# Kernel optimization log

Hardware: AMD Instinct MI355X
Metric: run time of the kernel (lower is better)

## Reference

```python
import jax, jax.numpy as jnp
import numpy as np

N_GROUP = 4
TOPK_GROUP = 2
TOP_K = 6
ROUTED_SCALE = 2.0

T, H, E, I = 1024, 1024, 16, 704
SHARED_I = 2 * H  # n_shared_experts * hidden_size


def setup_inputs() -> dict:
    key = jax.random.key(0)
    ks = jax.random.split(key, 10)
    s = 0.02
    return {
        "h": jax.random.normal(ks[0], (T, H), jnp.float32),
        "gate_w": jax.random.normal(ks[1], (E, H), jnp.float32) * s,
        "bias": jax.random.normal(ks[2], (E,), jnp.float32) * 0.1,
        "wg": jax.random.normal(ks[3], (E, H, I), jnp.float32) * s,
        "wu": jax.random.normal(ks[4], (E, H, I), jnp.float32) * s,
        "wd": jax.random.normal(ks[5], (E, I, H), jnp.float32) * s,
        "swg": jax.random.normal(ks[6], (H, SHARED_I), jnp.float32) * s,
        "swu": jax.random.normal(ks[7], (H, SHARED_I), jnp.float32) * s,
        "swd": jax.random.normal(ks[8], (SHARED_I, H), jnp.float32) * s,
    }


def _moe_forward(h, gate_w, bias, wg, wu, wd, swg, swu, swd):
    Tn, Hd = h.shape
    En = gate_w.shape[0]
    per_group = En // N_GROUP

    # shared expert (SwiGLU MLP)
    shared = (jax.nn.silu(h @ swg) * (h @ swu)) @ swd  # [T, H]

    # gate: noaux_tc biased grouped top-k routing (DeepSeek-V3 style)
    logits = h @ gate_w.T                      # [T, E]
    scores = jax.nn.sigmoid(logits)            # [T, E]
    scores_for_choice = scores + bias[None, :]
    grp = scores_for_choice.reshape(Tn, N_GROUP, per_group)
    group_scores = jnp.sum(jax.lax.top_k(grp, 2)[0], axis=-1)   # [T, G] top-2 sum
    _, top_groups = jax.lax.top_k(group_scores, TOPK_GROUP)     # [T, TG]
    gmask = jnp.zeros((Tn, N_GROUP), bool).at[
        jnp.arange(Tn)[:, None], top_groups].set(True)
    emask = jnp.repeat(gmask, per_group, axis=1)                # [T, E]
    masked = jnp.where(emask, scores_for_choice, -jnp.inf)
    _, topk_ids = jax.lax.top_k(masked, TOP_K)                  # [T, K]
    topk_w = jnp.take_along_axis(scores, topk_ids, axis=1)      # weights from unbiased scores
    topk_w = topk_w / jnp.sum(topk_w, axis=-1, keepdims=True)   # norm_topk_prob=True

    # sparse combine weights [T, E]
    cw = jnp.zeros((Tn, En), h.dtype).at[
        jnp.arange(Tn)[:, None], topk_ids].add(topk_w)

    # per-expert SwiGLU MLPs (dense over experts, sparse combine)
    g = jnp.einsum('th,ehi->tei', h, wg)
    u = jnp.einsum('th,ehi->tei', h, wu)
    y = jnp.einsum('tei,eih->teh', jax.nn.silu(g) * u, wd)
    routed = jnp.einsum('te,teh->th', cw, y)

    return routed * ROUTED_SCALE + shared


def reference(h, gate_w, bias, wg, wu, wd, swg, swu, swd):
    return _moe_forward(h, gate_w, bias, wg, wu, wd, swg, swu, swd)
```

## Files before the change

### kernel.cpp

```cpp
#include <hip/hip_runtime.h>
#include <hip/hip_bf16.h>
#include <math.h>

#define TT 1024
#define HH 1024
#define NEXP 16
#define NI 704
#define SI 2048
#define UPMAX 949
#define WDTILES 2816
#define DNSHARED 64
#define DNMAX (DNSHARED + 504)

typedef unsigned short us;
typedef __attribute__((ext_vector_type(8))) __bf16 bf16x8;
typedef __attribute__((ext_vector_type(4))) float f32x4;
typedef __attribute__((ext_vector_type(4))) unsigned short us4;

__device__ __forceinline__ us f2bf(float f) {
  unsigned u = __builtin_bit_cast(unsigned, f);
  u += 0x7fffu + ((u >> 16) & 1u);
  return (us)(u >> 16);
}

__device__ __forceinline__ int ldsOff(int row, int kg) {
  return (row * 4 + (kg ^ ((row >> 1) & 3))) * 16;
}

__device__ __forceinline__ void gl16(const void* g, void* l) {
  __builtin_amdgcn_global_load_lds((const __attribute__((address_space(1))) void*)g,
                                   (__attribute__((address_space(3))) void*)l, 16, 0, 0);
}

__device__ __forceinline__ int chunkMap(int b, int n) {
  int q = n >> 3, r = n & 7;
  int c = b & 7, i = b >> 3;
  int base = (c < r) ? c * (q + 1) : r * (q + 1) + (c - r) * q;
  return base + i;
}

__device__ __forceinline__ void tconv_tile(const float* __restrict__ inz,
                                           us* __restrict__ outz,
                                           int C, int ldo, int r0, int c0,
                                           float (*tile)[65]) {
  int t = threadIdx.x;
  int rr = t >> 4, cc = (t & 15) * 4;
  #pragma unroll
  for (int i = 0; i < 4; ++i) {
    f32x4 v = *reinterpret_cast<const f32x4*>(inz + (size_t)(r0 + rr + i * 16) * C + c0 + cc);
    tile[rr + i*16][cc + 0] = v[0];
    tile[rr + i*16][cc + 1] = v[1];
    tile[rr + i*16][cc + 2] = v[2];
    tile[rr + i*16][cc + 3] = v[3];
  }
  __syncthreads();
  int c = t >> 2, rq = t & 3;
  us o0[8], o1[8];
  #pragma unroll
  for (int j = 0; j < 8; ++j) {
    o0[j] = f2bf(tile[rq * 16 + j][c]);
    o1[j] = f2bf(tile[rq * 16 + 8 + j][c]);
  }
  us* op = outz + (size_t)(c0 + c) * ldo + r0 + rq * 16;
  *reinterpret_cast<us4*>(op)      = *reinterpret_cast<us4*>(&o0[0]);
  *reinterpret_cast<us4*>(op + 4)  = *reinterpret_cast<us4*>(&o0[4]);
  *reinterpret_cast<us4*>(op + 8)  = *reinterpret_cast<us4*>(&o1[0]);
  *reinterpret_cast<us4*>(op + 12) = *reinterpret_cast<us4*>(&o1[4]);
}

__global__ __launch_bounds__(256) void k_prep(
    const float* __restrict__ h, const float* __restrict__ gw,
    const float* __restrict__ bias, float* __restrict__ cw,
    us* __restrict__ hb, unsigned* __restrict__ selpk,
    const float* __restrict__ wg, const float* __restrict__ wu,
    const float* __restrict__ swg, const float* __restrict__ swu,
    us* __restrict__ wgb, us* __restrict__ wub,
    us* __restrict__ swgb, us* __restrict__ swub) {
  __shared__ float tile[64][65];
  __shared__ float lgS[NEXP];
  int b = blockIdx.x;
  int tid = threadIdx.x;
  if (b < 1024) {
    int t = b;
    const float* hr = h + (size_t)t * HH;
    {
      f32x4 v = *reinterpret_cast<const f32x4*>(hr + tid * 4);
      us4 p;
      p[0] = f2bf(v[0]); p[1] = f2bf(v[1]); p[2] = f2bf(v[2]); p[3] = f2bf(v[3]);
      *reinterpret_cast<us4*>(hb + (size_t)t * HH + tid * 4) = p;
    }
    int e = tid >> 4, sub = tid & 15;
    const f32x4* hr4 = reinterpret_cast<const f32x4*>(hr);
    const f32x4* gr4 = reinterpret_cast<const f32x4*>(gw + (size_t)e * HH);
    float acc = 0.f;
    for (int i = sub; i < 256; i += 16) {
      f32x4 a = hr4[i], g = gr4[i];
      acc += a[0]*g[0] + a[1]*g[1] + a[2]*g[2] + a[3]*g[3];
    }
    acc += __shfl_down(acc, 8, 16);
    acc += __shfl_down(acc, 4, 16);
    acc += __shfl_down(acc, 2, 16);
    acc += __shfl_down(acc, 1, 16);
    if (sub == 0) lgS[e] = acc;
    __syncthreads();
    if (tid == 0) {
      float sc[NEXP], s4[NEXP];
      for (int i = 0; i < NEXP; ++i) {
        sc[i] = 1.f / (1.f + expf(-lgS[i]));
        s4[i] = sc[i] + bias[i];
      }
      float gs[4];
      for (int g = 0; g < 4; ++g) {
        float a = s4[4*g], bb = s4[4*g+1], c = s4[4*g+2], d = s4[4*g+3];
        float mx01 = fmaxf(a, bb), mn01 = fminf(a, bb);
        float mx23 = fmaxf(c, d), mn23 = fminf(c, d);
        float top = fmaxf(mx01, mx23);
        float sec = (mx01 >= mx23) ? fmaxf(mn01, mx23) : fmaxf(mn23, mx01);
        gs[g] = top + sec;
      }
      int g1 = 0;
      for (int g = 1; g < 4; ++g) if (gs[g] > gs[g1]) g1 = g;
      int g2 = -1;
      for (int g = 0; g < 4; ++g) { if (g == g1) continue; if (g2 < 0 || gs[g] > gs[g2]) g2 = g; }
      int sel[6];
      bool used[NEXP];
      for (int i = 0; i < NEXP; ++i) used[i] = false;
      float wsum = 0.f;
      for (int it = 0; it < 6; ++it) {
        int best = -1; float bv = 0.f;
        for (int i = 0; i < NEXP; ++i) {
          int grp = i >> 2;
          if ((grp != g1 && grp != g2) || used[i]) continue;
          if (best < 0 || s4[i] > bv) { best = i; bv = s4[i]; }
        }
        used[best] = true;
        sel[it] = best;
        wsum += sc[best];
      }
      float inv = 2.0f / wsum;
      unsigned pk = 0;
      for (int it = 0; it < 6; ++it) {
        pk |= (unsigned)sel[it] << (it * 4);
        cw[(size_t)t * NEXP + sel[it]] = sc[sel[it]] * inv;
      }
      selpk[t] = pk;
    }
    return;
  }
  b -= 1024;
  if (b < 2816) {
    int z = b / 176, r = b % 176;
    tconv_tile(wg + (size_t)z * HH * NI, wgb + (size_t)z * NI * HH,
               NI, HH, (r / 11) * 64, (r % 11) * 64, tile);
    return;
  }
  b -= 2816;
  if (b < 2816) {
    int z = b / 176, r = b % 176;
    tconv_tile(wu + (size_t)z * HH * NI, wub + (size_t)z * NI * HH,
               NI, HH, (r / 11) * 64, (r % 11) * 64, tile);
    return;
  }
  b -= 2816;
  if (b < 512) {
    tconv_tile(swg, swgb, SI, HH, (b >> 5) * 64, (b & 31) * 64, tile);
    return;
  }
  b -= 512;
  {
    tconv_tile(swu, swub, SI, HH, (b >> 5) * 64, (b & 31) * 64, tile);
  }
}

__global__ void k_scan(const unsigned* __restrict__ selpk,
                       int* __restrict__ cnt, int* __restrict__ list,
                       int* __restrict__ wlUp, int* __restrict__ wlDn,
                       int* __restrict__ totals) {
  int t = threadIdx.x;
  int w = t >> 6, l = t & 63;
  unsigned pk = selpk[t];
  unsigned short flags = 0;
  #pragma unroll
  for (int j = 0; j < 6; ++j) flags |= (unsigned short)(1u << ((pk >> (j * 4)) & 15));
  __shared__ int wc[16][16];
  __shared__ int pre[16][16];
  __shared__ int tiles_s[16], upo[16], dno[16], totR[2];
  #pragma unroll
  for (int e = 0; e < 16; ++e) {
    unsigned long long bal = __ballot((flags >> e) & 1);
    if (l == 0) wc[w][e] = __popcll(bal);
  }
  __syncthreads();
  if (t < 16) {
    int s = 0;
    for (int ww = 0; ww < 16; ++ww) { pre[ww][t] = s; s += wc[ww][t]; }
    cnt[t] = s;
    tiles_s[t] = (s + 127) >> 7;
  }
  __syncthreads();
  if (t < 16) {
    int uo = 0, dn = 0;
    for (int e2 = 0; e2 < t; ++e2) { uo += 11 * tiles_s[e2]; dn += 8 * tiles_s[e2]; }
    upo[t] = uo; dno[t] = dn;
    if (t == 15) { totR[0] = uo + 11 * tiles_s[15]; totR[1] = dn + 8 * tiles_s[15]; }
  }
  __syncthreads();
  {
    int te = tiles_s[w];
    for (int i = l; i < 11 * te; i += 64) {
      int nt = i / te, mt = i - nt * te;
      wlUp[upo[w] + i] = ((w * 11 + nt) << 3) | mt;
    }
    for (int i = l; i < 8 * te; i += 64) {
      int nt = i / te, mt = i - nt * te;
      wlDn[dno[w] + i] = ((w * 8 + nt) << 3) | mt;
    }
  }
  if (w == 0) {
    for (int j = l; j < 256; j += 64)
      wlUp[totR[0] + j] = ((176 + (j >> 3)) << 3) | (j & 7);
  }
  if (t == 0) { totals[0] = totR[0] + 256; totals[1] = totR[1]; }
  unsigned long long lmask = (l == 0) ? 0ull : ((~0ull) >> (64 - l));
  #pragma unroll
  for (int e = 0; e < 16; ++e) {
    bool f = (flags >> e) & 1;
    unsigned long long bal = __ballot(f);
    if (f) {
      int rank = __popcll(bal & lmask);
      int j = 0;
      #pragma unroll
      for (int jj = 0; jj < 6; ++jj) j += (((pk >> (jj * 4)) & 15) == (unsigned)e) ? jj : 0;
      list[(e << 10) + pre[w][e] + rank] = (t << 3) | j;
    }
  }
}

__global__ void k_tconvS(const float* __restrict__ swd, us* __restrict__ swdT) {
  __shared__ float tile[64][65];
  int b = blockIdx.x;
  tconv_tile(swd, swdT, HH, SI, (b >> 4) * 64, (b & 15) * 64, tile);
}

__global__ __launch_bounds__(256) void k_upT(
    const us* __restrict__ hb,
    const us* __restrict__ wgb, const us* __restrict__ wub,
    const us* __restrict__ swgb, const us* __restrict__ swub,
    const float* __restrict__ cw, const int* __restrict__ list,
    const int* __restrict__ cnt, const int* __restrict__ wlUp,
    const int* __restrict__ totals,
    us* __restrict__ cact_r, us* __restrict__ cact_s,
    const float* __restrict__ wd, us* __restrict__ wdbT) {
  __shared__ __align__(16) char ldsb[32768];
  int tid = threadIdx.x;
  if ((int)blockIdx.x >= UPMAX) {
    int b = blockIdx.x - UPMAX;
    int z = b / 176, r = b % 176;
    tconv_tile(wd + (size_t)z * NI * HH, wdbT + (size_t)z * HH * NI,
               HH, NI, (r / 16) * 64, (r % 16) * 64,
               reinterpret_cast<float(*)[65]>(ldsb));
    return;
  }
  int tot = totals[0];
  if ((int)blockIdx.x >= tot) return;
  int item = wlUp[chunkMap(blockIdx.x, tot)];
  int group = item >> 3, mt = item & 7;
  int t0 = mt * 128;
  bool routed = group < 176;
  int e = 0, n0, cntE = TT;
  const us *bgBase, *buBase;
  if (routed) {
    e = group / 11;
    n0 = (group - e * 11) * 64;
    cntE = cnt[e];
    bgBase = wgb + (size_t)e * NI * HH;
    buBase = wub + (size_t)e * NI * HH;
  } else {
    n0 = (group - 176) * 64;
    bgBase = swgb;
    buBase = swub;
  }
  int w = tid >> 6, l = tid & 63;
  int wm = w >> 1, wn = w & 1;
  int lr = l & 15, lg2 = l >> 4;

  int rowA = tid >> 2;
  int kg = (tid & 3) ^ ((rowA >> 1) & 3);
  int tok0 = t0 + rowA, tok1 = t0 + 64 + rowA;
  if (routed) {
    tok0 = (tok0 < cntE) ? (list[(e << 10) + tok0] >> 3) : 0;
    tok1 = (tok1 < cntE) ? (list[(e << 10) + tok1] >> 3) : 0;
  }
  const us* aS0 = hb + (size_t)tok0 * HH + kg * 8;
  const us* aS1 = hb + (size_t)tok1 * HH + kg * 8;
  const us* gS  = bgBase + (size_t)(n0 + rowA) * HH + kg * 8;
  const us* uS  = buBase + (size_t)(n0 + rowA) * HH + kg * 8;

  f32x4 accG[4][2] = {};
  f32x4 accU[4][2] = {};

  int wslot = w * 1024;
  auto stage = [&](char* buf) {
    char* b = buf + wslot;
    gl16(aS0, b);
    gl16(aS1, b + 4096);
    gl16(gS,  b + 8192);
    gl16(uS,  b + 12288);
    aS0 += 32; aS1 += 32; gS += 32; uS += 32;
  };

  char* bufR = ldsb;
  char* bufW = ldsb + 16384;
  stage(bufR);
  __syncthreads();
  #pragma unroll 2
  for (int ki = 0; ki < 32; ++ki) {
    if (ki < 31) stage(bufW);
    bf16x8 af[4], bg[2], bu[2];
    #pragma unroll
    for (int rf = 0; rf < 4; ++rf)
      af[rf] = *reinterpret_cast<const bf16x8*>(bufR + ldsOff(wm * 64 + rf * 16 + lr, lg2));
    #pragma unroll
    for (int cf = 0; cf < 2; ++cf) {
      int n = wn * 32 + cf * 16 + lr;
      bg[cf] = *reinterpret_cast<const bf16x8*>(bufR + 8192  + ldsOff(n, lg2));
      bu[cf] = *reinterpret_cast<const bf16x8*>(bufR + 12288 + ldsOff(n, lg2));
    }
    #pragma unroll
    for (int rf = 0; rf < 4; ++rf)
      #pragma unroll
      for (int cf = 0; cf < 2; ++cf) {
        accG[rf][cf] = __builtin_amdgcn_mfma_f32_16x16x32_bf16(af[rf], bg[cf], accG[rf][cf], 0, 0, 0);
        accU[rf][cf] = __builtin_amdgcn_mfma_f32_16x16x32_bf16(af[rf], bu[cf], accU[rf][cf], 0, 0, 0);
      }
    __syncthreads();
    char* tp = bufR; bufR = bufW; bufW = tp;
  }
  #pragma unroll
  for (int rf = 0; rf < 4; ++rf)
    #pragma unroll
    for (int cf = 0; cf < 2; ++cf)
      #pragma unroll
      for (int r = 0; r < 4; ++r) {
        int row = wm * 64 + rf * 16 + lg2 * 4 + r;
        int col = wn * 32 + cf * 16 + lr;
        float g = accG[rf][cf][r], u = accU[rf][cf][r];
        float act = g / (1.f + __expf(-g)) * u;
        if (routed) {
          int slot = t0 + row;
          if (slot < cntE) {
            int packed = list[(e << 10) + slot];
            float scl = cw[(size_t)(packed >> 3) * NEXP + e];
            cact_r[((size_t)(e << 10) + slot) * NI + n0 + col] = f2bf(act * scl);
          }
        } else {
          cact_s[(size_t)(t0 + row) * SI + n0 + col] = f2bf(act);
        }
      }
}

__global__ __launch_bounds__(256) void k_down(
    const us* __restrict__ cact_r, const us* __restrict__ cact_s,
    const us* __restrict__ wdbT, const us* __restrict__ swdT,
    const int* __restrict__ list, const int* __restrict__ cnt,
    const int* __restrict__ wlDn, const int* __restrict__ totals,
    us* __restrict__ part, float* __restrict__ out) {
  __shared__ __align__(16) char ldsb[32768];
  int tid = threadIdx.x;
  int b = blockIdx.x;
  bool routed;
  int e = 0, nt, mt, kiter, Ksrc, cntE = TT;
  const us *Ab, *Bb;
  if (b < DNSHARED) {
    routed = false;
    nt = b & 7;
    mt = b >> 3;
    kiter = 64;
    Ksrc = SI;
    Ab = cact_s;
    Bb = swdT;
  } else {
    routed = true;
    int rb = b - DNSHARED;
    int tot = totals[1];
    if (rb >= tot) return;
    int item = wlDn[chunkMap(rb, tot)];
    int group = item >> 3;
    mt = item & 7;
    e = group >> 3; nt = group & 7;
    cntE = cnt[e];
    kiter = NI / 32;
    Ksrc = NI;
    Ab = cact_r + (size_t)e * 1024 * NI;
    Bb = wdbT + (size_t)e * 1024 * NI;
  }
  int t0 = mt * 128;
  int n0 = nt * 128;
  int w = tid >> 6, l = tid & 63;
  int wm = w >> 1, wn = w & 1;
  int lr = l & 15, lg2 = l >> 4;

  int rowA = tid >> 2;
  int kg = (tid & 3) ^ ((rowA >> 1) & 3);
  const us* aS0 = Ab + (size_t)(t0 + rowA) * Ksrc + kg * 8;
  const us* aS1 = Ab + (size_t)(t0 + 64 + rowA) * Ksrc + kg * 8;
  const us* bS0 = Bb + (size_t)(n0 + rowA) * Ksrc + kg * 8;
  const us* bS1 = Bb + (size_t)(n0 + 64 + rowA) * Ksrc + kg * 8;

  f32x4 acc[4][4] = {};

  int wslot = w * 1024;
  auto stage = [&](char* buf) {
    char* bp = buf + wslot;
    gl16(aS0, bp);
    gl16(aS1, bp + 4096);
    gl16(bS0, bp + 8192);
    gl16(bS1, bp + 12288);
    aS0 += 32; aS1 += 32; bS0 += 32; bS1 += 32;
  };

  char* bufR = ldsb;
  char* bufW = ldsb + 16384;
  stage(bufR);
  __syncthreads();
  for (int ki = 0; ki < kiter; ++ki) {
    if (ki + 1 < kiter) stage(bufW);
    bf16x8 af[4], bb[4];
    #pragma unroll
    for (int rf = 0; rf < 4; ++rf)
      af[rf] = *reinterpret_cast<const bf16x8*>(bufR + ldsOff(wm * 64 + rf * 16 + lr, lg2));
    #pragma unroll
    for (int cf = 0; cf < 4; ++cf)
      bb[cf] = *reinterpret_cast<const bf16x8*>(bufR + 8192 + ldsOff(wn * 64 + cf * 16 + lr, lg2));
    #pragma unroll
    for (int rf = 0; rf < 4; ++rf)
      #pragma unroll
      for (int cf = 0; cf < 4; ++cf)
        acc[rf][cf] = __builtin_amdgcn_mfma_f32_16x16x32_bf16(af[rf], bb[cf], acc[rf][cf], 0, 0, 0);
    __syncthreads();
    char* tp = bufR; bufR = bufW; bufW = tp;
  }
  #pragma unroll
  for (int rf = 0; rf < 4; ++rf)
    #pragma unroll
    for (int cf = 0; cf < 4; ++cf)
      #pragma unroll
      for (int r = 0; r < 4; ++r) {
        int row = wm * 64 + rf * 16 + lg2 * 4 + r;
        int col = wn * 64 + cf * 16 + lr;
        if (routed) {
          int slot = t0 + row;
          if (slot < cntE) {
            int packed = list[(e << 10) + slot];
            int t = packed >> 3, j = packed & 7;
            part[((size_t)t * 6 + j) * 1024 + n0 + col] = f2bf(acc[rf][cf][r]);
          }
        } else {
          out[(size_t)(t0 + row) * HH + n0 + col] = acc[rf][cf][r];
        }
      }
}

__global__ void k_reduce(const us* __restrict__ part, float* __restrict__ out) {
  int i = (blockIdx.x * blockDim.x + threadIdx.x) * 4;
  int t = i >> 10, hh = i & 1023;
  f32x4 s = *reinterpret_cast<const f32x4*>(out + i);
  #pragma unroll
  for (int j = 0; j < 6; ++j) {
    us4 p = *reinterpret_cast<const us4*>(part + ((size_t)t * 6 + j) * 1024 + hh);
    #pragma unroll
    for (int k = 0; k < 4; ++k)
      s[k] += __builtin_bit_cast(float, (unsigned)p[k] << 16);
  }
  *reinterpret_cast<f32x4*>(out + i) = s;
}

#define HB_OFF    0ULL
#define CW_OFF    2097152ULL
#define CNT_OFF   2162688ULL
#define SELPK_OFF 2166784ULL
#define LIST_OFF  2170880ULL
#define WLUP_OFF  2236416ULL
#define WLDN_OFF  2244608ULL
#define TOT_OFF   2252800ULL
#define CACTR_OFF 2260992ULL
#define CACTS_OFF 25329664ULL
#define WGB_OFF   29523968ULL
#define WUB_OFF   52592640ULL
#define SWGB_OFF  75661312ULL
#define SWUB_OFF  79855616ULL
#define WDBT_OFF  84049920ULL
#define SWDT_OFF  SWGB_OFF
#define PART_OFF  WGB_OFF

extern "C" void kernel_launch(void* const* d_in, const int* in_sizes, int n_in,
                              void* d_out, int out_size, void* d_ws, size_t ws_size,
                              hipStream_t stream) {
  const float* h    = (const float*)d_in[0];
  const float* gw   = (const float*)d_in[1];
  const float* bias = (const float*)d_in[2];
  const float* wg   = (const float*)d_in[3];
  const float* wu   = (const float*)d_in[4];
  const float* wd   = (const float*)d_in[5];
  const float* swg  = (const float*)d_in[6];
  const float* swu  = (const float*)d_in[7];
  const float* swd  = (const float*)d_in[8];
  float* out = (float*)d_out;

  char* ws = (char*)d_ws;
  us*       hb     = (us*)(ws + HB_OFF);
  float*    cw     = (float*)(ws + CW_OFF);
  int*      cnt    = (int*)(ws + CNT_OFF);
  unsigned* selpk  = (unsigned*)(ws + SELPK_OFF);
  int*      list   = (int*)(ws + LIST_OFF);
  int*      wlUp   = (int*)(ws + WLUP_OFF);
  int*      wlDn   = (int*)(ws + WLDN_OFF);
  int*      totals = (int*)(ws + TOT_OFF);
  us*       cact_r = (us*)(ws + CACTR_OFF);
  us*       cact_s = (us*)(ws + CACTS_OFF);
  us*       wgb    = (us*)(ws + WGB_OFF);
  us*       wub    = (us*)(ws + WUB_OFF);
  us*       swgb   = (us*)(ws + SWGB_OFF);
  us*       swub   = (us*)(ws + SWUB_OFF);
  us*       wdbT   = (us*)(ws + WDBT_OFF);
  us*       swdT   = (us*)(ws + SWDT_OFF);
  us*       part   = (us*)(ws + PART_OFF);

  k_prep<<<7680, 256, 0, stream>>>(h, gw, bias, cw, hb, selpk,
                                   wg, wu, swg, swu, wgb, wub, swgb, swub);
  k_scan<<<1, 1024, 0, stream>>>(selpk, cnt, list, wlUp, wlDn, totals);

  k_upT<<<UPMAX + WDTILES, 256, 0, stream>>>(hb, wgb, wub, swgb, swub, cw, list,
                                             cnt, wlUp, totals, cact_r, cact_s,
                                             wd, wdbT);

  k_tconvS<<<512, 256, 0, stream>>>(swd, swdT);

  k_down<<<DNMAX, 256, 0, stream>>>(cact_r, cact_s, wdbT, swdT, list, cnt,
                                    wlDn, totals, part, out);
  k_reduce<<<1024, 256, 0, stream>>>(part, out);
}
```

Baseline: 156.7 us.

## Widen up-projection tile to 128x128 with 512-thread blocks

The gate/up GEMM blocks move from 128x64 to 128x128 output tiles with 8 waves. The work list now covers 6 column tiles per expert, padding the last one past 704 with a clamped row and a guarded store. The bundled wd transpose path also processes 64x128 tiles per block. The aim is more reuse of the gathered token rows and fewer blocks, at the cost of wasted work in the padded tile and higher LDS use per block.

```diff
diff --git a/kernel.cpp b/kernel.cpp
--- a/kernel.cpp
+++ b/kernel.cpp
@@ -7,8 +7,8 @@
 #define NEXP 16
 #define NI 704
 #define SI 2048
-#define UPMAX 949
-#define WDTILES 2816
+#define UPMAX 506
+#define WDTILES 1408
 #define DNSHARED 64
 #define DNMAX (DNSHARED + 504)
 
@@ -66,6 +66,31 @@
   *reinterpret_cast<us4*>(op + 4)  = *reinterpret_cast<us4*>(&o0[4]);
   *reinterpret_cast<us4*>(op + 8)  = *reinterpret_cast<us4*>(&o1[0]);
   *reinterpret_cast<us4*>(op + 12) = *reinterpret_cast<us4*>(&o1[4]);
+}
+
+__device__ __forceinline__ void tconv512(const float* __restrict__ inz,
+                                         us* __restrict__ outz,
+                                         int i0, int h0, float (*tile)[129]) {
+  int t = threadIdx.x;
+  int ir = t >> 3, cg = (t & 7) * 4;
+  #pragma unroll
+  for (int p = 0; p < 4; ++p) {
+    f32x4 v = *reinterpret_cast<const f32x4*>(inz + (size_t)(i0 + ir) * HH + h0 + cg + p * 32);
+    tile[ir][cg + p*32 + 0] = v[0];
+    tile[ir][cg + p*32 + 1] = v[1];
+    tile[ir][cg + p*32 + 2] = v[2];
+    tile[ir][cg + p*32 + 3] = v[3];
+  }
+  __syncthreads();
+  int c = t >> 2, rq = t & 3;
+  us o[16];
+  #pragma unroll
+  for (int j = 0; j < 16; ++j) o[j] = f2bf(tile[rq * 16 + j][c]);
+  us* op = outz + (size_t)(h0 + c) * NI + i0 + rq * 16;
+  *reinterpret_cast<us4*>(op)      = *reinterpret_cast<us4*>(&o[0]);
+  *reinterpret_cast<us4*>(op + 4)  = *reinterpret_cast<us4*>(&o[4]);
+  *reinterpret_cast<us4*>(op + 8)  = *reinterpret_cast<us4*>(&o[8]);
+  *reinterpret_cast<us4*>(op + 12) = *reinterpret_cast<us4*>(&o[12]);
 }
 
 __global__ __launch_bounds__(256) void k_prep(
@@ -200,16 +225,16 @@
   __syncthreads();
   if (t < 16) {
     int uo = 0, dn = 0;
-    for (int e2 = 0; e2 < t; ++e2) { uo += 11 * tiles_s[e2]; dn += 8 * tiles_s[e2]; }
+    for (int e2 = 0; e2 < t; ++e2) { uo += 6 * tiles_s[e2]; dn += 8 * tiles_s[e2]; }
     upo[t] = uo; dno[t] = dn;
-    if (t == 15) { totR[0] = uo + 11 * tiles_s[15]; totR[1] = dn + 8 * tiles_s[15]; }
+    if (t == 15) { totR[0] = uo + 6 * tiles_s[15]; totR[1] = dn + 8 * tiles_s[15]; }
   }
   __syncthreads();
   {
     int te = tiles_s[w];
-    for (int i = l; i < 11 * te; i += 64) {
+    for (int i = l; i < 6 * te; i += 64) {
       int nt = i / te, mt = i - nt * te;
-      wlUp[upo[w] + i] = ((w * 11 + nt) << 3) | mt;
+      wlUp[upo[w] + i] = ((w * 6 + nt) << 3) | mt;
     }
     for (int i = l; i < 8 * te; i += 64) {
       int nt = i / te, mt = i - nt * te;
@@ -217,10 +242,10 @@
     }
   }
   if (w == 0) {
-    for (int j = l; j < 256; j += 64)
-      wlUp[totR[0] + j] = ((176 + (j >> 3)) << 3) | (j & 7);
-  }
-  if (t == 0) { totals[0] = totR[0] + 256; totals[1] = totR[1]; }
+    for (int j = l; j < 128; j += 64)
+      wlUp[totR[0] + j] = ((96 + (j >> 3)) << 3) | (j & 7);
+  }
+  if (t == 0) { totals[0] = totR[0] + 128; totals[1] = totR[1]; }
   unsigned long long lmask = (l == 0) ? 0ull : ((~0ull) >> (64 - l));
   #pragma unroll
   for (int e = 0; e < 16; ++e) {
@@ -242,7 +267,7 @@
   tconv_tile(swd, swdT, HH, SI, (b >> 4) * 64, (b & 15) * 64, tile);
 }
 
-__global__ __launch_bounds__(256) void k_upT(
+__global__ __launch_bounds__(512) void k_upT(
     const us* __restrict__ hb,
     const us* __restrict__ wgb, const us* __restrict__ wub,
     const us* __restrict__ swgb, const us* __restrict__ swub,
@@ -251,14 +276,14 @@
     const int* __restrict__ totals,
     us* __restrict__ cact_r, us* __restrict__ cact_s,
     const float* __restrict__ wd, us* __restrict__ wdbT) {
-  __shared__ __align__(16) char ldsb[32768];
+  __shared__ __align__(16) char ldsb[49152];
   int tid = threadIdx.x;
   if ((int)blockIdx.x >= UPMAX) {
     int b = blockIdx.x - UPMAX;
-    int z = b / 176, r = b % 176;
-    tconv_tile(wd + (size_t)z * NI * HH, wdbT + (size_t)z * HH * NI,
-               HH, NI, (r / 16) * 64, (r % 16) * 64,
-               reinterpret_cast<float(*)[65]>(ldsb));
+    int z = b / 88, r = b % 88;
+    tconv512(wd + (size_t)z * NI * HH, wdbT + (size_t)z * HH * NI,
+             (r >> 3) * 64, (r & 7) * 128,
+             reinterpret_cast<float(*)[129]>(ldsb));
     return;
   }
   int tot = totals[0];
@@ -266,35 +291,33 @@
   int item = wlUp[chunkMap(blockIdx.x, tot)];
   int group = item >> 3, mt = item & 7;
   int t0 = mt * 128;
-  bool routed = group < 176;
+  bool routed = group < 96;
   int e = 0, n0, cntE = TT;
   const us *bgBase, *buBase;
   if (routed) {
-    e = group / 11;
-    n0 = (group - e * 11) * 64;
+    e = group / 6;
+    n0 = (group - e * 6) * 128;
     cntE = cnt[e];
     bgBase = wgb + (size_t)e * NI * HH;
     buBase = wub + (size_t)e * NI * HH;
   } else {
-    n0 = (group - 176) * 64;
+    n0 = (group - 96) * 128;
     bgBase = swgb;
     buBase = swub;
   }
   int w = tid >> 6, l = tid & 63;
-  int wm = w >> 1, wn = w & 1;
+  int wm = w >> 2, wn = w & 3;
   int lr = l & 15, lg2 = l >> 4;
 
   int rowA = tid >> 2;
   int kg = (tid & 3) ^ ((rowA >> 1) & 3);
-  int tok0 = t0 + rowA, tok1 = t0 + 64 + rowA;
-  if (routed) {
-    tok0 = (tok0 < cntE) ? (list[(e << 10) + tok0] >> 3) : 0;
-    tok1 = (tok1 < cntE) ? (list[(e << 10) + tok1] >> 3) : 0;
-  }
-  const us* aS0 = hb + (size_t)tok0 * HH + kg * 8;
-  const us* aS1 = hb + (size_t)tok1 * HH + kg * 8;
-  const us* gS  = bgBase + (size_t)(n0 + rowA) * HH + kg * 8;
-  const us* uS  = buBase + (size_t)(n0 + rowA) * HH + kg * 8;
+  int tok = t0 + rowA;
+  if (routed) tok = (tok < cntE) ? (list[(e << 10) + tok] >> 3) : 0;
+  int bRow = n0 + rowA;
+  if (routed && bRow >= NI) bRow = NI - 1;
+  const us* aS = hb + (size_t)tok * HH + kg * 8;
+  const us* gS = bgBase + (size_t)bRow * HH + kg * 8;
+  const us* uS = buBase + (size_t)bRow * HH + kg * 8;
 
   f32x4 accG[4][2] = {};
   f32x4 accU[4][2] = {};
@@ -302,15 +325,14 @@
   int wslot = w * 1024;
   auto stage = [&](char* buf) {
     char* b = buf + wslot;
-    gl16(aS0, b);
-    gl16(aS1, b + 4096);
-    gl16(gS,  b + 8192);
-    gl16(uS,  b + 12288);
-    aS0 += 32; aS1 += 32; gS += 32; uS += 32;
+    gl16(aS, b);
+    gl16(gS, b + 8192);
+    gl16(uS, b + 16384);
+    aS += 32; gS += 32; uS += 32;
   };
 
   char* bufR = ldsb;
-  char* bufW = ldsb + 16384;
+  char* bufW = ldsb + 24576;
   stage(bufR);
   __syncthreads();
   #pragma unroll 2
@@ -324,7 +346,7 @@
     for (int cf = 0; cf < 2; ++cf) {
       int n = wn * 32 + cf * 16 + lr;
       bg[cf] = *reinterpret_cast<const bf16x8*>(bufR + 8192  + ldsOff(n, lg2));
-      bu[cf] = *reinterpret_cast<const bf16x8*>(bufR + 12288 + ldsOff(n, lg2));
+      bu[cf] = *reinterpret_cast<const bf16x8*>(bufR + 16384 + ldsOff(n, lg2));
     }
     #pragma unroll
     for (int rf = 0; rf < 4; ++rf)
@@ -348,7 +370,7 @@
         float act = g / (1.f + __expf(-g)) * u;
         if (routed) {
           int slot = t0 + row;
-          if (slot < cntE) {
+          if (slot < cntE && n0 + col < NI) {
             int packed = list[(e << 10) + slot];
             float scl = cw[(size_t)(packed >> 3) * NEXP + e];
             cact_r[((size_t)(e << 10) + slot) * NI + n0 + col] = f2bf(act * scl);
@@ -530,7 +552,7 @@
                                    wg, wu, swg, swu, wgb, wub, swgb, swub);
   k_scan<<<1, 1024, 0, stream>>>(selpk, cnt, list, wlUp, wlDn, totals);
 
-  k_upT<<<UPMAX + WDTILES, 256, 0, stream>>>(hb, wgb, wub, swgb, swub, cw, list,
+  k_upT<<<UPMAX + WDTILES, 512, 0, stream>>>(hb, wgb, wub, swgb, swub, cw, list,
                                              cnt, wlUp, totals, cact_r, cact_s,
                                              wd, wdbT);
 
```

New measurement: 138.9 us. 11.4% less time.
